# Performance work log

Measured on AMD Instinct MI355X. Metric: run time of the kernel, lower is better.

## Reference

```python
import jax, jax.numpy as jnp
import numpy as np
from jax import lax

DILATIONS = [1, 2, 4, 8, 16, 32, 64, 128, 256, 512]
KERNEL = 3
CH = 64
B, T = 8, 16384
L = len(DILATIONS)


def setup_inputs() -> dict:
    key = jax.random.key(0)
    ks = jax.random.split(key, 5)
    x = jax.random.normal(ks[0], (B, CH, T), dtype=jnp.float32)
    # gated conv: out_channels = 2*CH (tanh half | sigmoid half)
    weights_conv = jax.random.normal(ks[1], (L, 2 * CH, CH, KERNEL), dtype=jnp.float32) * 0.1
    biases_conv = jax.random.normal(ks[2], (L, 2 * CH), dtype=jnp.float32) * 0.1
    weights_out = jax.random.normal(ks[3], (L, CH, CH), dtype=jnp.float32) * 0.1
    biases_out = jax.random.normal(ks[4], (L, CH), dtype=jnp.float32) * 0.1
    return {
        "x": x,
        "weights_conv": weights_conv,
        "biases_conv": biases_conv,
        "weights_out": weights_out,
        "biases_out": biases_out,
    }


def _stack_forward(x, weights_conv, biases_conv, weights_out, biases_out):
    skips = []
    for i, d in enumerate(DILATIONS):
        h = x  # residual branch
        pad = (KERNEL - 1) * d  # causal left padding
        y = lax.conv_general_dilated(
            x, weights_conv[i],
            window_strides=(1,), padding=[(pad, 0)], rhs_dilation=(d,),
            dimension_numbers=("NCH", "OIH", "NCH"),
        ) + biases_conv[i][None, :, None]
        yt, ys = jnp.split(y, 2, axis=1)          # gated activation
        a = jnp.tanh(yt) * jax.nn.sigmoid(ys)      # (B, CH, T)
        skips.append(a)                            # skip = activation output
        if i < L - 1:  # last layer has use_output_transform=False
            out = jnp.einsum("oc,bct->bot", weights_out[i], a) + biases_out[i][None, :, None]
        else:
            out = a
        x = out + h  # residual add
    # pack (output, skips[0..L-1]) into one array of shape (L+1, B, CH, T)
    return jnp.concatenate([x[None], jnp.stack(skips, axis=0)], axis=0)


def reference(x, weights_conv, biases_conv, weights_out, biases_out):
    return _stack_forward(x, weights_conv, biases_conv, weights_out, biases_out)
```

## Files before the change

### kernel.cpp

```cpp
#include <hip/hip_runtime.h>
#include <hip/hip_bf16.h>


#define CH 64
#define TLEN 16384
#define NB 8
#define BN 128
#define NLAYER 10

typedef __attribute__((ext_vector_type(4))) float f32x4;
typedef __attribute__((ext_vector_type(8))) short s16x8;
typedef __attribute__((ext_vector_type(4))) unsigned short u16x4;

__device__ __forceinline__ unsigned short f2bf(float f) {
    union { float f; unsigned u; } v; v.f = f;
    unsigned r = v.u + 0x7fffu + ((v.u >> 16) & 1u);
    return (unsigned short)(r >> 16);
}
__device__ __forceinline__ float bf2f(unsigned short u) {
    union { unsigned u; float f; } v; v.u = ((unsigned)u) << 16;
    return v.f;
}
__device__ __forceinline__ void gload_lds16(const void* g, void* l) {
    __builtin_amdgcn_global_load_lds(
        (const __attribute__((address_space(1))) unsigned int*)g,
        (__attribute__((address_space(3))) unsigned int*)l, 16, 0, 0);
}

#define NCONV (NLAYER * 4 * 2 * 6 * 64 * 8)
#define NOUT  (NLAYER * 4 * 2 * 64 * 8)

__global__ void pack_weights(const float* __restrict__ wconv,
                             const float* __restrict__ wout,
                             unsigned short* __restrict__ wcpk,
                             unsigned short* __restrict__ wopk)
{
    int idx = blockIdx.x * 256 + threadIdx.x;
    if (idx < NCONV) {
        int j = idx & 7, t = idx >> 3;
        int lane = t & 63; t >>= 6;
        int ks = t % 6;   t /= 6;
        int m  = t & 1;   t >>= 1;
        int wv = t & 3;   int l = t >> 2;
        int o  = (m * 4 + wv) * 16 + (lane & 15);
        int ck = ks * 32 + (lane >> 4) * 8 + j;
        int kk = ck >> 6, c = ck & 63;
        wcpk[idx] = f2bf(wconv[(((size_t)l * 128 + o) * CH + c) * 3 + (2 - kk)]);
    } else if (idx < NCONV + NOUT) {
        int id = idx - NCONV;
        int j = id & 7, t = id >> 3;
        int lane = t & 63; t >>= 6;
        int ks = t & 1;    t >>= 1;
        int wv = t & 3;    int l = t >> 2;
        int o  = wv * 16 + (lane & 15);
        int c  = ks * 32 + (lane >> 4) * 8 + j;
        wopk[id] = f2bf(wout[((size_t)l * CH + o) * CH + c]);
    }
}

template<int SM, bool LAST>
__global__ __launch_bounds__(256, 3)
void wavenet_layer(const void* __restrict__ xin_, void* __restrict__ xout_,
                   float* __restrict__ skip,
                   const unsigned short* __restrict__ wcpk,
                   const unsigned short* __restrict__ wopk,
                   const float* __restrict__ bconv, const float* __restrict__ bout,
                   int layer, int dil)
{
    extern __shared__ __align__(16) unsigned short xs[];
    unsigned short* as_ = xs;

    const int tid  = threadIdx.x;
    const int lane = tid & 63;
    const int wv   = tid >> 6;
    const int hrow = lane & 15;
    const int kgrp = lane >> 4;
    const int b  = blockIdx.y;
    const int t0 = blockIdx.x * BN;
    const int NW = BN + 2 * dil;
    const size_t xbase = (size_t)b * CH * TLEN;

    if (SM == 0) {
        const float* xin = (const float*)xin_;
        #pragma unroll
        for (int c8 = 0; c8 < 8; ++c8) {
            for (int np = tid; np < NW; np += 256) {
                const int tg = t0 - 2 * dil + np;
                s16x8 pk = {0, 0, 0, 0, 0, 0, 0, 0};
                if (tg >= 0) {
                    const float* p = xin + xbase + (size_t)(c8 * 8) * TLEN + tg;
                    #pragma unroll
                    for (int j = 0; j < 8; ++j) pk[j] = (short)f2bf(p[(size_t)j * TLEN]);
                }
                *reinterpret_cast<s16x8*>(&xs[(size_t)(c8 * NW + np) * 8]) = pk;
            }
        }
    } else if (SM == 1) {
        const unsigned short* xin = (const unsigned short*)xin_;
        const int cnt_n = (NW + 63) >> 6;
        if (t0 >= 2 * dil) {
            for (int ch = wv; ch < 8 * cnt_n; ch += 4) {
                const int c8 = ch / cnt_n;
                const int n0 = (ch % cnt_n) * 64;
                const int rem = NW - n0;
                const unsigned short* src =
                    xin + xbase + (size_t)(t0 - 2 * dil + n0 + lane) * CH + c8 * 8;
                unsigned short* dst = &xs[(size_t)(c8 * NW + n0) * 8];
                if (rem >= 64) gload_lds16(src, dst);
                else if (lane < rem) gload_lds16(src, dst);
            }
        } else {
            for (int ch = wv; ch < 8 * cnt_n; ch += 4) {
                const int c8 = ch / cnt_n;
                const int n0 = (ch % cnt_n) * 64;
                if (n0 + lane < NW) {
                    const int tg = t0 - 2 * dil + n0 + lane;
                    s16x8 pk = {0, 0, 0, 0, 0, 0, 0, 0};
                    if (tg >= 0)
                        pk = *reinterpret_cast<const s16x8*>(xin + xbase + (size_t)tg * CH + c8 * 8);
                    *reinterpret_cast<s16x8*>(&xs[(size_t)(c8 * NW + n0 + lane) * 8]) = pk;
                }
            }
        }
    } else {
        const unsigned short* xin = (const unsigned short*)xin_;
        if (t0 >= 2 * dil) {
            for (int ch = wv; ch < 48; ch += 4) {
                const int kk = ch >> 4, c8 = (ch >> 1) & 7, n0 = (ch & 1) * 64;
                const unsigned short* src =
                    xin + xbase + (size_t)(t0 + n0 + lane - kk * dil) * CH + c8 * 8;
                unsigned short* dst = &xs[(size_t)((kk * 8 + c8) * BN + n0) * 8];
                gload_lds16(src, dst);
            }
        } else {
            for (int ch = wv; ch < 48; ch += 4) {
                const int kk = ch >> 4, c8 = (ch >> 1) & 7, n0 = (ch & 1) * 64;
                const int tg = t0 + n0 + lane - kk * dil;
                s16x8 pk = {0, 0, 0, 0, 0, 0, 0, 0};
                if (tg >= 0)
                    pk = *reinterpret_cast<const s16x8*>(xin + xbase + (size_t)tg * CH + c8 * 8);
                *reinterpret_cast<s16x8*>(&xs[(size_t)((kk * 8 + c8) * BN + n0 + lane) * 8]) = pk;
            }
        }
    }

    s16x8 wa[2][6];
    {
        const unsigned short* base = wcpk + ((size_t)(layer * 4 + wv) * 768 + lane) * 8;
        #pragma unroll
        for (int m = 0; m < 2; ++m)
            #pragma unroll
            for (int ks = 0; ks < 6; ++ks)
                wa[m][ks] = *reinterpret_cast<const s16x8*>(base + (size_t)(m * 6 + ks) * 512);
    }
    const float* Bc = bconv + (size_t)layer * 128;
    float bt[4], bs[4];
    #pragma unroll
    for (int r = 0; r < 4; ++r) {
        bt[r] = Bc[wv * 16 + kgrp * 4 + r];
        bs[r] = Bc[64 + wv * 16 + kgrp * 4 + r];
    }

    __syncthreads();

    f32x4 accT[8], accS[8];
    #pragma unroll
    for (int nt = 0; nt < 8; ++nt) {
        accT[nt] = (f32x4){0.f, 0.f, 0.f, 0.f};
        accS[nt] = (f32x4){0.f, 0.f, 0.f, 0.f};
    }
    #pragma unroll
    for (int nt = 0; nt < 8; ++nt) {
        #pragma unroll
        for (int ks = 0; ks < 6; ++ks) {
            const int kb = ks * 4 + kgrp;
            const unsigned short* bp;
            if (SM == 2) {
                bp = &xs[(size_t)(kb * BN + nt * 16 + hrow) * 8];
            } else {
                const int kk = kb >> 3, c8i = kb & 7;
                bp = &xs[(size_t)(c8i * NW + nt * 16 + hrow + (2 - kk) * dil) * 8];
            }
            const s16x8 bf = *reinterpret_cast<const s16x8*>(bp);
            accT[nt] = __builtin_amdgcn_mfma_f32_16x16x32_bf16(wa[0][ks], bf, accT[nt], 0, 0, 0);
            accS[nt] = __builtin_amdgcn_mfma_f32_16x16x32_bf16(wa[1][ks], bf, accS[nt], 0, 0, 0);
        }
    }

    if (!LAST) __syncthreads();

    #pragma unroll
    for (int nt = 0; nt < 8; ++nt) {
        #pragma unroll
        for (int r = 0; r < 4; ++r) {
            const float yt = accT[nt][r] + bt[r];
            const float ys = accS[nt][r] + bs[r];
            const float th = 2.f * __builtin_amdgcn_rcpf(1.f + __expf(-2.f * yt)) - 1.f;
            const float sg = __builtin_amdgcn_rcpf(1.f + __expf(-ys));
            const float av = th * sg;
            const int c = wv * 16 + kgrp * 4 + r;
            const int n = nt * 16 + hrow;
            skip[xbase + (size_t)c * TLEN + t0 + n] = av;
            if (LAST) {
                const float res = bf2f(xs[(size_t)((c >> 3) * BN + n) * 8 + (c & 7)]);
                ((float*)xout_)[xbase + (size_t)c * TLEN + t0 + n] = av + res;
            } else {
                as_[(size_t)((c >> 3) * BN + n) * 8 + (c & 7)] = f2bf(av);
            }
        }
    }

    if (LAST) return;

    __syncthreads();

    const unsigned short* b2 = wopk + ((size_t)(layer * 4 + wv) * 128 + lane) * 8;
    s16x8 wa2[2];
    wa2[0] = *reinterpret_cast<const s16x8*>(b2);
    wa2[1] = *reinterpret_cast<const s16x8*>(b2 + 512);
    const float* Bo = bout + (size_t)layer * CH;
    float bo[4];
    #pragma unroll
    for (int r = 0; r < 4; ++r) bo[r] = Bo[wv * 16 + kgrp * 4 + r];

    const int o0 = wv * 16 + kgrp * 4;
    unsigned short* xout = (unsigned short*)xout_;

    #pragma unroll
    for (int nt = 0; nt < 8; ++nt) {
        f32x4 acc = (f32x4){0.f, 0.f, 0.f, 0.f};
        #pragma unroll
        for (int ks = 0; ks < 2; ++ks) {
            const s16x8 bf = *reinterpret_cast<const s16x8*>(
                &as_[(size_t)((ks * 4 + kgrp) * BN + nt * 16 + hrow) * 8]);
            acc = __builtin_amdgcn_mfma_f32_16x16x32_bf16(wa2[ks], bf, acc, 0, 0, 0);
        }
        const int n = nt * 16 + hrow;
        float res[4];
        if (SM == 0) {
            const float* xin = (const float*)xin_;
            #pragma unroll
            for (int r = 0; r < 4; ++r)
                res[r] = xin[xbase + (size_t)(o0 + r) * TLEN + t0 + n];
        } else {
            const u16x4 rv = *reinterpret_cast<const u16x4*>(
                (const unsigned short*)xin_ + xbase + (size_t)(t0 + n) * CH + o0);
            #pragma unroll
            for (int r = 0; r < 4; ++r) res[r] = bf2f(rv[r]);
        }
        u16x4 ov;
        #pragma unroll
        for (int r = 0; r < 4; ++r) ov[r] = f2bf(acc[r] + bo[r] + res[r]);
        *reinterpret_cast<u16x4*>(&xout[xbase + (size_t)(t0 + n) * CH + o0]) = ov;
    }
}

extern "C" void kernel_launch(void* const* d_in, const int* in_sizes, int n_in,
                              void* d_out, int out_size, void* d_ws, size_t ws_size,
                              hipStream_t stream)
{
    const float* x  = (const float*)d_in[0];
    const float* wc = (const float*)d_in[1];
    const float* bc = (const float*)d_in[2];
    const float* wo = (const float*)d_in[3];
    const float* bo = (const float*)d_in[4];
    float* out = (float*)d_out;
    const size_t planeF  = (size_t)NB * CH * TLEN;
    const size_t planeBy = planeF * sizeof(unsigned short);

    unsigned short* P0 = (unsigned short*)d_ws;
    unsigned short* P1 = (unsigned short*)((char*)d_ws + planeBy);
    unsigned short* wcpk = (unsigned short*)((char*)d_ws + 2 * planeBy);
    unsigned short* wopk = wcpk + NCONV;

    pack_weights<<<(NCONV + NOUT) / 256, 256, 0, stream>>>(wc, wo, wcpk, wopk);

    dim3 grid(TLEN / BN, NB), block(256);

    wavenet_layer<0, false><<<grid, block, 130 * 128, stream>>>(
        x, P0, out + planeF, wcpk, wopk, bc, bo, 0, 1);

    for (int i = 1; i < NLAYER - 1; ++i) {
        const int d = 1 << i;
        const void* xi = (i & 1) ? (void*)P0 : (void*)P1;
        void* xo = (i & 1) ? (void*)P1 : (void*)P0;
        float* skip = out + (size_t)(1 + i) * planeF;
        if (d <= 64)
            wavenet_layer<1, false><<<grid, block, (size_t)(BN + 2 * d) * 128, stream>>>(
                xi, xo, skip, wcpk, wopk, bc, bo, i, d);
        else
            wavenet_layer<2, false><<<grid, block, 24 * BN * 8 * 2, stream>>>(
                xi, xo, skip, wcpk, wopk, bc, bo, i, d);
    }

    wavenet_layer<2, true><<<grid, block, 24 * BN * 8 * 2, stream>>>(
        P0, out, out + (size_t)NLAYER * planeF, wcpk, wopk, bc, bo, 9, 512);
}
```

Baseline: 250.3 us.

## Fuse first five dilated layers into one kernel with LDS-resident halo

Adds a head kernel that loads a 192-sample window (a 64-sample halo plus the 128-sample tile) of the input once. It then runs layers 0–4 entirely in shared memory, ping-ponging the residual plane and recomputing the halo region at each layer. This removes four kernel launches and four round trips of the bf16 intermediate plane through global memory. In exchange it does redundant conv work on the halo (192 vs 128 columns), holds many accumulators per thread (which may cause register spills), and launches at lower occupancy.

```diff
diff --git a/kernel.cpp b/kernel.cpp
--- a/kernel.cpp
+++ b/kernel.cpp
@@ -7,6 +7,10 @@
 #define NB 8
 #define BN 128
 #define NLAYER 10
+
+#define WP   192
+#define PSTR 194
+#define ASTR 130
 
 typedef __attribute__((ext_vector_type(4))) float f32x4;
 typedef __attribute__((ext_vector_type(8))) short s16x8;
@@ -58,6 +62,189 @@
     }
 }
 
+__global__ __launch_bounds__(256, 2)
+void wavenet_head(const float* __restrict__ x, unsigned short* __restrict__ xplane,
+                  float* __restrict__ out,
+                  const unsigned short* __restrict__ wcpk,
+                  const unsigned short* __restrict__ wopk,
+                  const float* __restrict__ bconv, const float* __restrict__ bout)
+{
+    __shared__ __align__(16) unsigned short pl[2][8 * PSTR * 8];
+    __shared__ __align__(16) unsigned short as_[8 * ASTR * 8];
+
+    const int tid  = threadIdx.x;
+    const int lane = tid & 63;
+    const int wv   = tid >> 6;
+    const int hrow = lane & 15;
+    const int kgrp = lane >> 4;
+    const int b  = blockIdx.y;
+    const int t0 = blockIdx.x * BN;
+    const size_t xbase  = (size_t)b * CH * TLEN;
+    const size_t planeF = (size_t)NB * CH * TLEN;
+
+    if (tid < WP) {
+        const int tt = t0 - 64 + tid;
+        #pragma unroll
+        for (int c8 = 0; c8 < 8; ++c8) {
+            s16x8 pk = {0, 0, 0, 0, 0, 0, 0, 0};
+            if (tt >= 0) {
+                const float* p = x + xbase + (size_t)(c8 * 8) * TLEN + tt;
+                #pragma unroll
+                for (int j = 0; j < 8; ++j) pk[j] = (short)f2bf(p[(size_t)j * TLEN]);
+            }
+            *reinterpret_cast<s16x8*>(&pl[0][(size_t)(c8 * PSTR + tid) * 8]) = pk;
+        }
+    }
+    __syncthreads();
+
+    int cur = 0;
+    for (int l = 0; l < 5; ++l) {
+        const int dil = 1 << l;
+        unsigned short* plc = pl[cur];
+        unsigned short* pln = pl[cur ^ 1];
+
+        s16x8 wa[2][6];
+        {
+            const unsigned short* basew = wcpk + ((size_t)(l * 4 + wv) * 768 + lane) * 8;
+            #pragma unroll
+            for (int m = 0; m < 2; ++m)
+                #pragma unroll
+                for (int ks = 0; ks < 6; ++ks)
+                    wa[m][ks] = *reinterpret_cast<const s16x8*>(basew + (size_t)(m * 6 + ks) * 512);
+        }
+        const float* Bc = bconv + (size_t)l * 128;
+        float bt[4], bs[4];
+        #pragma unroll
+        for (int r = 0; r < 4; ++r) {
+            bt[r] = Bc[wv * 16 + kgrp * 4 + r];
+            bs[r] = Bc[64 + wv * 16 + kgrp * 4 + r];
+        }
+        s16x8 wa2[2];
+        {
+            const unsigned short* b2 = wopk + ((size_t)(l * 4 + wv) * 128 + lane) * 8;
+            wa2[0] = *reinterpret_cast<const s16x8*>(b2);
+            wa2[1] = *reinterpret_cast<const s16x8*>(b2 + 512);
+        }
+        const float* Bo = bout + (size_t)l * CH;
+        float bo[4];
+        #pragma unroll
+        for (int r = 0; r < 4; ++r) bo[r] = Bo[wv * 16 + kgrp * 4 + r];
+
+        f32x4 accT[12], accS[12];
+        #pragma unroll
+        for (int nt = 0; nt < 12; ++nt) {
+            accT[nt] = (f32x4){0.f, 0.f, 0.f, 0.f};
+            accS[nt] = (f32x4){0.f, 0.f, 0.f, 0.f};
+        }
+        #pragma unroll
+        for (int nt = 0; nt < 12; ++nt) {
+            #pragma unroll
+            for (int ks = 0; ks < 6; ++ks) {
+                const int kb = ks * 4 + kgrp;
+                const int kk = kb >> 3, c8i = kb & 7;
+                int q = nt * 16 + hrow - kk * dil;
+                if (q < 0) q = 0;
+                const s16x8 bf = *reinterpret_cast<const s16x8*>(&plc[(size_t)(c8i * PSTR + q) * 8]);
+                accT[nt] = __builtin_amdgcn_mfma_f32_16x16x32_bf16(wa[0][ks], bf, accT[nt], 0, 0, 0);
+                accS[nt] = __builtin_amdgcn_mfma_f32_16x16x32_bf16(wa[1][ks], bf, accS[nt], 0, 0, 0);
+            }
+        }
+
+        float* skipl = out + (size_t)(1 + l) * planeF + xbase;
+        const int o0 = wv * 16 + kgrp * 4;
+
+        #pragma unroll
+        for (int nt = 0; nt < 8; ++nt) {
+            #pragma unroll
+            for (int r = 0; r < 4; ++r) {
+                const float yt = accT[nt][r] + bt[r];
+                const float ys = accS[nt][r] + bs[r];
+                const float th = 2.f * __builtin_amdgcn_rcpf(1.f + __expf(-2.f * yt)) - 1.f;
+                const float sg = __builtin_amdgcn_rcpf(1.f + __expf(-ys));
+                const float av = th * sg;
+                const int c = wv * 16 + kgrp * 4 + r;
+                const int p = nt * 16 + hrow;
+                if (nt >= 4) skipl[(size_t)c * TLEN + t0 + p - 64] = av;
+                as_[(size_t)((c >> 3) * ASTR + p) * 8 + (c & 7)] = f2bf(av);
+            }
+        }
+        __syncthreads();
+        #pragma unroll
+        for (int nt = 0; nt < 8; ++nt) {
+            f32x4 a2 = (f32x4){0.f, 0.f, 0.f, 0.f};
+            const int p = nt * 16 + hrow;
+            #pragma unroll
+            for (int ks2 = 0; ks2 < 2; ++ks2) {
+                const s16x8 bf = *reinterpret_cast<const s16x8*>(
+                    &as_[(size_t)((ks2 * 4 + kgrp) * ASTR + p) * 8]);
+                a2 = __builtin_amdgcn_mfma_f32_16x16x32_bf16(wa2[ks2], bf, a2, 0, 0, 0);
+            }
+            const int tt = t0 - 64 + p;
+            const u16x4 rv = *reinterpret_cast<const u16x4*>(
+                &plc[(size_t)((o0 >> 3) * PSTR + p) * 8 + (o0 & 7)]);
+            if (l == 4) {
+                if (nt >= 4) {
+                    u16x4 ov;
+                    #pragma unroll
+                    for (int r = 0; r < 4; ++r) ov[r] = f2bf(a2[r] + bo[r] + bf2f(rv[r]));
+                    *reinterpret_cast<u16x4*>(&xplane[xbase + (size_t)tt * CH + o0]) = ov;
+                }
+            } else {
+                u16x4 ov;
+                #pragma unroll
+                for (int r = 0; r < 4; ++r)
+                    ov[r] = (tt >= 0) ? f2bf(a2[r] + bo[r] + bf2f(rv[r])) : (unsigned short)0;
+                *reinterpret_cast<u16x4*>(&pln[(size_t)((o0 >> 3) * PSTR + p) * 8 + (o0 & 7)]) = ov;
+            }
+        }
+        __syncthreads();
+        #pragma unroll
+        for (int nt = 8; nt < 12; ++nt) {
+            #pragma unroll
+            for (int r = 0; r < 4; ++r) {
+                const float yt = accT[nt][r] + bt[r];
+                const float ys = accS[nt][r] + bs[r];
+                const float th = 2.f * __builtin_amdgcn_rcpf(1.f + __expf(-2.f * yt)) - 1.f;
+                const float sg = __builtin_amdgcn_rcpf(1.f + __expf(-ys));
+                const float av = th * sg;
+                const int c = wv * 16 + kgrp * 4 + r;
+                const int p = nt * 16 + hrow;
+                skipl[(size_t)c * TLEN + t0 + p - 64] = av;
+                as_[(size_t)((c >> 3) * ASTR + p - 128) * 8 + (c & 7)] = f2bf(av);
+            }
+        }
+        __syncthreads();
+        #pragma unroll
+        for (int nt = 8; nt < 12; ++nt) {
+            f32x4 a2 = (f32x4){0.f, 0.f, 0.f, 0.f};
+            const int p = nt * 16 + hrow;
+            #pragma unroll
+            for (int ks2 = 0; ks2 < 2; ++ks2) {
+                const s16x8 bf = *reinterpret_cast<const s16x8*>(
+                    &as_[(size_t)((ks2 * 4 + kgrp) * ASTR + p - 128) * 8]);
+                a2 = __builtin_amdgcn_mfma_f32_16x16x32_bf16(wa2[ks2], bf, a2, 0, 0, 0);
+            }
+            const int tt = t0 - 64 + p;
+            const u16x4 rv = *reinterpret_cast<const u16x4*>(
+                &plc[(size_t)((o0 >> 3) * PSTR + p) * 8 + (o0 & 7)]);
+            if (l == 4) {
+                u16x4 ov;
+                #pragma unroll
+                for (int r = 0; r < 4; ++r) ov[r] = f2bf(a2[r] + bo[r] + bf2f(rv[r]));
+                *reinterpret_cast<u16x4*>(&xplane[xbase + (size_t)tt * CH + o0]) = ov;
+            } else {
+                u16x4 ov;
+                #pragma unroll
+                for (int r = 0; r < 4; ++r) ov[r] = f2bf(a2[r] + bo[r] + bf2f(rv[r]));
+                *reinterpret_cast<u16x4*>(&pln[(size_t)((o0 >> 3) * PSTR + p) * 8 + (o0 & 7)]) = ov;
+            }
+        }
+        __syncthreads();
+
+        cur ^= 1;
+    }
+}
+
 template<int SM, bool LAST>
 __global__ __launch_bounds__(256, 3)
 void wavenet_layer(const void* __restrict__ xin_, void* __restrict__ xout_,
@@ -80,22 +267,7 @@
     const int NW = BN + 2 * dil;
     const size_t xbase = (size_t)b * CH * TLEN;
 
-    if (SM == 0) {
-        const float* xin = (const float*)xin_;
-        #pragma unroll
-        for (int c8 = 0; c8 < 8; ++c8) {
-            for (int np = tid; np < NW; np += 256) {
-                const int tg = t0 - 2 * dil + np;
-                s16x8 pk = {0, 0, 0, 0, 0, 0, 0, 0};
-                if (tg >= 0) {
-                    const float* p = xin + xbase + (size_t)(c8 * 8) * TLEN + tg;
-                    #pragma unroll
-                    for (int j = 0; j < 8; ++j) pk[j] = (short)f2bf(p[(size_t)j * TLEN]);
-                }
-                *reinterpret_cast<s16x8*>(&xs[(size_t)(c8 * NW + np) * 8]) = pk;
-            }
-        }
-    } else if (SM == 1) {
+    if (SM == 1) {
         const unsigned short* xin = (const unsigned short*)xin_;
         const int cnt_n = (NW + 63) >> 6;
         if (t0 >= 2 * dil) {
@@ -236,21 +408,11 @@
             acc = __builtin_amdgcn_mfma_f32_16x16x32_bf16(wa2[ks], bf, acc, 0, 0, 0);
         }
         const int n = nt * 16 + hrow;
-        float res[4];
-        if (SM == 0) {
-            const float* xin = (const float*)xin_;
-            #pragma unroll
-            for (int r = 0; r < 4; ++r)
-                res[r] = xin[xbase + (size_t)(o0 + r) * TLEN + t0 + n];
-        } else {
-            const u16x4 rv = *reinterpret_cast<const u16x4*>(
-                (const unsigned short*)xin_ + xbase + (size_t)(t0 + n) * CH + o0);
-            #pragma unroll
-            for (int r = 0; r < 4; ++r) res[r] = bf2f(rv[r]);
-        }
+        const u16x4 rv = *reinterpret_cast<const u16x4*>(
+            (const unsigned short*)xin_ + xbase + (size_t)(t0 + n) * CH + o0);
         u16x4 ov;
         #pragma unroll
-        for (int r = 0; r < 4; ++r) ov[r] = f2bf(acc[r] + bo[r] + res[r]);
+        for (int r = 0; r < 4; ++r) ov[r] = f2bf(acc[r] + bo[r] + bf2f(rv[r]));
         *reinterpret_cast<u16x4*>(&xout[xbase + (size_t)(t0 + n) * CH + o0]) = ov;
     }
 }
@@ -277,22 +439,16 @@
 
     dim3 grid(TLEN / BN, NB), block(256);
 
-    wavenet_layer<0, false><<<grid, block, 130 * 128, stream>>>(
-        x, P0, out + planeF, wcpk, wopk, bc, bo, 0, 1);
-
-    for (int i = 1; i < NLAYER - 1; ++i) {
-        const int d = 1 << i;
-        const void* xi = (i & 1) ? (void*)P0 : (void*)P1;
-        void* xo = (i & 1) ? (void*)P1 : (void*)P0;
-        float* skip = out + (size_t)(1 + i) * planeF;
-        if (d <= 64)
-            wavenet_layer<1, false><<<grid, block, (size_t)(BN + 2 * d) * 128, stream>>>(
-                xi, xo, skip, wcpk, wopk, bc, bo, i, d);
-        else
-            wavenet_layer<2, false><<<grid, block, 24 * BN * 8 * 2, stream>>>(
-                xi, xo, skip, wcpk, wopk, bc, bo, i, d);
-    }
-
+    wavenet_head<<<grid, block, 0, stream>>>(x, P0, out, wcpk, wopk, bc, bo);
+
+    wavenet_layer<1, false><<<grid, block, (size_t)(BN + 64) * 128, stream>>>(
+        P0, P1, out + 6 * planeF, wcpk, wopk, bc, bo, 5, 32);
+    wavenet_layer<1, false><<<grid, block, (size_t)(BN + 128) * 128, stream>>>(
+        P1, P0, out + 7 * planeF, wcpk, wopk, bc, bo, 6, 64);
+    wavenet_layer<2, false><<<grid, block, 24 * BN * 8 * 2, stream>>>(
+        P0, P1, out + 8 * planeF, wcpk, wopk, bc, bo, 7, 128);
+    wavenet_layer<2, false><<<grid, block, 24 * BN * 8 * 2, stream>>>(
+        P1, P0, out + 9 * planeF, wcpk, wopk, bc, bo, 8, 256);
     wavenet_layer<2, true><<<grid, block, 24 * BN * 8 * 2, stream>>>(
-        P0, out, out + (size_t)NLAYER * planeF, wcpk, wopk, bc, bo, 9, 512);
-}
+        P0, out, out + 10 * planeF, wcpk, wopk, bc, bo, 9, 512);
+}
```

Measured after the change: 248.2 us. No clear change (-0.8%).
